# Optimization experiments

Hardware: AMD Instinct MI355X
Metric: run time of the kernel (lower is better)

## Reference

```python
import jax, jax.numpy as jnp
from jax import lax
import numpy as np

B = 32  # batch


def _conv(x, w, b, pad):
    # x: [B,Cin,H,W], w: [Cout,Cin,kh,kw], b: [Cout]
    y = lax.conv_general_dilated(x, w, window_strides=(1, 1), padding=pad,
                                 dimension_numbers=("NCHW", "OIHW", "NCHW"))
    return y + b[None, :, None, None]


def setup_inputs() -> dict:
    keys = jax.random.split(jax.random.key(0), 16)
    ki = iter(keys)
    f32 = jnp.float32

    def W(shape):
        return jax.random.normal(next(ki), shape, f32) * 0.05

    return {
        "x": jax.random.normal(next(ki), (B, 64, 64), f32),
        # 64 independent spatial convs per stage, each Conv2d(Cin,31,(64,3))
        "W1": W((64, 31, 1, 64, 3)),  "b1": jnp.zeros((64, 31), f32),
        "W2": W((64, 31, 31, 64, 3)), "b2": jnp.zeros((64, 31), f32),
        "W3": W((64, 31, 31, 64, 3)), "b3": jnp.zeros((64, 31), f32),
        # 2 edge spectral stacks: Conv(2,64,9)->ReLU->Conv(64,32,1)->ReLU->Conv(32,1,5)
        "We1a": W((2, 64, 2, 9, 9)),  "be1a": jnp.zeros((2, 64), f32),
        "We1b": W((2, 32, 64, 1, 1)), "be1b": jnp.zeros((2, 32), f32),
        "We1c": W((2, 1, 32, 5, 5)),  "be1c": jnp.zeros((2, 1), f32),
        # 29 interior spectral stacks: Conv(3,64,9)->ReLU->Conv(64,32,1)->ReLU->Conv(32,1,5)
        "We2a": W((29, 64, 3, 9, 9)),  "be2a": jnp.zeros((29, 64), f32),
        "We2b": W((29, 32, 64, 1, 1)), "be2b": jnp.zeros((29, 32), f32),
        "We2c": W((29, 1, 32, 5, 5)),  "be2c": jnp.zeros((29, 1), f32),
    }


def _spatial(inp, Ws, bs):
    # inp: [B,Cin,64,64]; Ws: [64,31,Cin,64,3]; bs: [64,31]
    def one(w, b):
        return jax.nn.relu(_conv(inp, w, b, [(0, 0), (1, 1)]))  # [B,31,1,64]
    rows = jax.vmap(one)(Ws, bs)            # [64,B,31,1,64]; row i = output line i
    return jnp.transpose(rows[:, :, :, 0, :], (1, 2, 0, 3))  # [B,31,64,64]


def _spectral(xin, wa, ba, wb, bb, wc, bc):
    h = jax.nn.relu(_conv(xin, wa, ba, [(4, 4), (4, 4)]))
    h = jax.nn.relu(_conv(h, wb, bb, [(0, 0), (0, 0)]))
    return _conv(h, wc, bc, [(2, 2), (2, 2)])[:, 0]  # [B,64,64]


def reference(x, W1, b1, W2, b2, W3, b3,
              We1a, be1a, We1b, be1b, We1c, be1c,
              We2a, be2a, We2b, be2b, We2c, be2c):
    xb = x[:, None]                         # [B,1,64,64]
    s1 = _spatial(xb, W1, b1)               # [B,31,64,64]
    s2 = _spatial(s1, W2, b2)
    s3 = _spatial(s2, W3, b3)

    # edge bands 0 and 30 use 2-channel slices
    edge_in = jnp.stack([s3[:, 0:2], s3[:, 29:31]])   # [2,B,2,64,64]
    edge = jax.vmap(_spectral)(edge_in, We1a, be1a, We1b, be1b, We1c, be1c)  # [2,B,64,64]

    # interior bands 1..29 use sliding 3-channel slices
    idx = jnp.arange(29)[:, None] + jnp.arange(3)[None, :]  # [29,3]
    mid_in = jnp.transpose(s3[:, idx], (1, 0, 2, 3, 4))     # [29,B,3,64,64]
    mid = jax.vmap(_spectral)(mid_in, We2a, be2a, We2b, be2b, We2c, be2c)  # [29,B,64,64]

    recon = jnp.concatenate(
        [edge[0][:, None], jnp.transpose(mid, (1, 0, 2, 3)), edge[1][:, None]], axis=1)
    out = s3 + recon                        # [B,31,64,64]
    # torch: .transpose(3,1).transpose(2,1) == permute(0,2,3,1)
    return jnp.transpose(out, (0, 2, 3, 1))  # [B,64,64,31]
```

## Files before the change

### kernel.cpp

```cpp
#include <hip/hip_runtime.h>
#include <hip/hip_bf16.h>
#include <stdint.h>

typedef unsigned short u16;
typedef unsigned int   u32;
typedef __attribute__((ext_vector_type(8))) short bf16x8;
typedef __attribute__((ext_vector_type(4))) float f32x4;

__device__ __forceinline__ float us2f(u16 u){ return __uint_as_float(((u32)u)<<16); }
__device__ __forceinline__ float lo2f(u32 w){ return __uint_as_float(w<<16); }
__device__ __forceinline__ float hi2f(u32 w){ return __uint_as_float(w & 0xffff0000u); }
__device__ __forceinline__ u16 f2us(float f){
  u32 u = __float_as_uint(f);
  u32 r = (u + 0x7FFFu + ((u>>16)&1u)) >> 16;
  return (u16)r;
}
__device__ __forceinline__ u32 pk2(float a, float b){ return (u32)f2us(a) | ((u32)f2us(b)<<16); }

__global__ __launch_bounds__(256) void k_prep_x(const float* __restrict__ x, u16* __restrict__ xT){
  __shared__ float tile[64][65];
  const int b = blockIdx.x, t = threadIdx.x;
  #pragma unroll
  for (int q=0;q<4;q++){
    int idx = q*256 + t, r = idx>>4, w4 = (idx&15)*4;
    float4 v = *(const float4*)&x[((size_t)b*64 + r)*64 + w4];
    tile[r][w4]=v.x; tile[r][w4+1]=v.y; tile[r][w4+2]=v.z; tile[r][w4+3]=v.w;
  }
  __syncthreads();
  #pragma unroll
  for (int q=0;q<2;q++){
    int idx = q*256 + t, w = idx>>3, rc = idx&7;
    uint4 o;
    o.x = pk2(tile[rc*8+0][w], tile[rc*8+1][w]);
    o.y = pk2(tile[rc*8+2][w], tile[rc*8+3][w]);
    o.z = pk2(tile[rc*8+4][w], tile[rc*8+5][w]);
    o.w = pk2(tile[rc*8+6][w], tile[rc*8+7][w]);
    *(uint4*)&xT[((size_t)b*64 + w)*64 + rc*8] = o;
  }
}

__global__ __launch_bounds__(256) void k_prep_w(const float* __restrict__ W,
        u16* __restrict__ Wp, int CI){
  __shared__ float rowW[5952];
  const int h = blockIdx.x, i = blockIdx.y, t = threadIdx.x;
  for (int idx=t; idx<1488; idx+=256){
    int o = idx/48, j4 = (idx - o*48)*4;
    float4 v = *(const float4*)&W[ (((size_t)h*31 + o)*CI + i)*192 + j4 ];
    *(float4*)&rowW[o*192 + j4] = v;
  }
  __syncthreads();
  for (int idx=t; idx<768; idx+=256){
    int dw = idx>>8, rem = idx&255, o = rem>>3, rc = rem&7;
    uint4 ov = {0,0,0,0};
    if (o < 31){
      const float* s = &rowW[o*192 + dw];
      ov.x = pk2(s[(rc*8+0)*3], s[(rc*8+1)*3]);
      ov.y = pk2(s[(rc*8+2)*3], s[(rc*8+3)*3]);
      ov.z = pk2(s[(rc*8+4)*3], s[(rc*8+5)*3]);
      ov.w = pk2(s[(rc*8+6)*3], s[(rc*8+7)*3]);
    }
    *(uint4*)&Wp[ ((((size_t)h*CI + i)*3 + dw)*32 + o)*64 + rc*8 ] = ov;
  }
}

__global__ __launch_bounds__(256) void k_tr(const u16* __restrict__ in, u16* __restrict__ outp){
  __shared__ u16 tile[64*72];
  const int b = blockIdx.x, o = blockIdx.y, t = threadIdx.x;
  const uint4* src = (const uint4*)(in + ((size_t)b*31 + o)*4096);
  #pragma unroll
  for (int q=0;q<2;q++){
    int idx = q*256 + t, hh = idx>>3, u = idx&7;
    *(uint4*)&tile[hh*72 + ((u ^ ((hh>>3)&7))*8)] = src[idx];
  }
  __syncthreads();
  u16* dst = outp + ((size_t)b*31 + o)*4096;
  #pragma unroll
  for (int q=0;q<2;q++){
    int idx = q*256 + t, w = idx>>3, hc = (idx&7)*8;
    u32 ow[4];
    #pragma unroll
    for (int j=0;j<4;j++){
      int h0 = hc + j*2, h1 = h0 + 1;
      u16 a = tile[h0*72 + (((w>>3) ^ ((h0>>3)&7))*8) + (w&7)];
      u16 bb= tile[h1*72 + (((w>>3) ^ ((h1>>3)&7))*8) + (w&7)];
      ow[j] = (u32)a | ((u32)bb<<16);
    }
    uint4 ov = {ow[0], ow[1], ow[2], ow[3]};
    *(uint4*)&dst[(size_t)w*64 + hc] = ov;
  }
}

__global__ __launch_bounds__(512) void k_spatial2(const u16* __restrict__ inT_g,
        const u16* __restrict__ Wp, const float* __restrict__ bias,
        float* __restrict__ outF, u16* __restrict__ outT, int CI, int mode){
  __shared__ __align__(16) u16 inT[2][66*72];
  const int t    = threadIdx.x;
  const int wv   = t>>6;
  const int lane = t&63;
  const int l15  = lane&15;
  const int quad = lane>>4;
  const int wg  = blockIdx.x;
  const int xcd = wg & 7;
  const int li  = wg >> 3;
  const int hg  = xcd*2 + (li>>5);
  const int b   = li & 31;
  const int h   = hg*4 + (wv&3);
  const int nho = wv>>2;

  if (t < 72){
    inT[0][t] = 0; inT[0][65*72 + t] = 0;
    inT[1][t] = 0; inT[1][65*72 + t] = 0;
  }

  f32x4 acc[4];
  #pragma unroll
  for (int ms=0;ms<4;ms++) acc[ms] = (f32x4){0.f,0.f,0.f,0.f};

  const uint4* srcb = (const uint4*)(inT_g + (size_t)b*CI*4096);
  const u16*   wr   = Wp + (size_t)h*CI*3*32*64;

  uint4 pf = srcb[t];
  bf16x8 bA[2][3], bB[2][3];
  #pragma unroll
  for (int dw=0;dw<3;dw++)
    #pragma unroll
    for (int kh=0;kh<2;kh++)
      bA[kh][dw] = *(const bf16x8*)&wr[(dw*32 + nho*16 + l15)*64 + kh*32 + quad*8];

  auto body = [&](bf16x8 (&bcur)[2][3], bf16x8 (&bnext)[2][3], int i){
    u16* L = inT[i&1];
    {
      int row = t>>3, ch = t&7;
      *(uint4*)&L[(row+1)*72 + ch*8] = pf;
    }
    int inext = (i+1 < CI) ? (i+1) : (CI-1);
    pf = (srcb + (size_t)inext*512)[t];
    const u16* wbase = wr + (size_t)inext*6144;
    #pragma unroll
    for (int dw=0;dw<3;dw++)
      #pragma unroll
      for (int kh=0;kh<2;kh++)
        bnext[kh][dw] = *(const bf16x8*)&wbase[(dw*32 + nho*16 + l15)*64 + kh*32 + quad*8];
    asm volatile("s_waitcnt lgkmcnt(0)" ::: "memory");
    __builtin_amdgcn_s_barrier();
    __builtin_amdgcn_sched_barrier(0);
    #pragma unroll
    for (int kh=0; kh<2; kh++){
      #pragma unroll
      for (int dw=0; dw<3; dw++){
        bf16x8 afr[4];
        #pragma unroll
        for (int ms=0;ms<4;ms++)
          afr[ms] = *(const bf16x8*)&L[(ms*16 + l15 + dw)*72 + kh*32 + quad*8];
        #pragma unroll
        for (int ms=0;ms<4;ms++)
          acc[ms] = __builtin_amdgcn_mfma_f32_16x16x32_bf16(afr[ms], bcur[kh][dw], acc[ms], 0,0,0);
      }
    }
  };

  int i = 0;
  while (true){
    body(bA, bB, i); if (++i >= CI) break;
    body(bB, bA, i); if (++i >= CI) break;
  }

  {
    int o = nho*16 + l15;
    if (o < 31){
      float bv = bias[h*31 + o];
      if (mode == 0){
        #pragma unroll
        for (int ms=0;ms<4;ms++){
          size_t base = (((size_t)b*31 + o)*64 + h)*64 + ms*16 + quad*4;
          #pragma unroll
          for (int reg=0;reg<4;reg++)
            outF[base + reg] = fmaxf(acc[ms][reg] + bv, 0.f);
        }
      } else {
        #pragma unroll
        for (int ms=0;ms<4;ms++){
          uint2 pw;
          pw.x = pk2(fmaxf(acc[ms][0] + bv, 0.f), fmaxf(acc[ms][1] + bv, 0.f));
          pw.y = pk2(fmaxf(acc[ms][2] + bv, 0.f), fmaxf(acc[ms][3] + bv, 0.f));
          *(uint2*)&outT[ (((size_t)b*31 + o)*64 + h)*64 + ms*16 + quad*4 ] = pw;
        }
      }
    }
  }
}

__global__ __launch_bounds__(256) void k_prep(
    const float* __restrict__ We1a, const float* __restrict__ We2a,
    const float* __restrict__ We1b, const float* __restrict__ We2b,
    u16* __restrict__ waP, u16* __restrict__ wbP){
  int t = blockIdx.x*256 + threadIdx.x;
  if (t < 17856){
    int g = t/576, rem = t - g*576, dx = rem>>6, c = rem&63;
    int C; const float* wa;
    if (g==0)      { C=2; wa = We1a; }
    else if (g==30){ C=2; wa = We1a + 64*2*81; }
    else           { C=3; wa = We2a + (size_t)(g-1)*64*3*81; }
    const float* wrow = wa + (size_t)c*C*81;
    u16* dst = waP + ((size_t)(g*9 + dx)*64 + c)*40;
    int Kr = C*9;
    for (int k=0;k<40;k++){
      u16 v = 0;
      if (k < Kr) v = f2us(wrow[k*9 + dx]);
      dst[k] = v;
    }
  } else if (t < 17856 + 992){
    int u = t - 17856; int g = u>>5, c2 = u&31;
    const float* wb;
    if (g==0)      wb = We1b;
    else if (g==30) wb = We1b + 32*64;
    else            wb = We2b + (size_t)(g-1)*32*64;
    u16* dst = wbP + ((size_t)g*32 + c2)*72;
    for (int k=0;k<64;k++) dst[k] = f2us(wb[c2*64 + k]);
    for (int k=64;k<72;k++) dst[k] = 0;
  }
}

__global__ __launch_bounds__(256) void k_spec_ab(
    const float* __restrict__ s3,
    const u16* __restrict__ waP, const u16* __restrict__ wbP,
    const float* __restrict__ be1a, const float* __restrict__ be1b,
    const float* __restrict__ be2a, const float* __restrict__ be2b,
    u16* __restrict__ hb, int g0){
  __shared__ __align__(16) unsigned char smem[36864];
  u16* colT  = (u16*)smem;
  u16* stage = (u16*)(smem + 23040);
  u16* haT   = (u16*)smem;
  u16* hbL   = (u16*)smem;

  const int t = threadIdx.x;
  const int yo = blockIdx.x, b = blockIdx.y;
  const int gl = blockIdx.z;
  const int g  = g0 + gl;
  const int y0 = yo*4;
  const int wv = t>>6, lane = t&63, l15 = lane&15, quad = lane>>4;

  int C, cb; const float *ba, *bb;
  if (g==0)      { C=2; cb=0;  ba=be1a;           bb=be1b;        }
  else if (g==30){ C=2; cb=29; ba=be1a+64;        bb=be1b+32;     }
  else           { C=3; cb=g-1; ba=be2a+(size_t)(g-1)*64; bb=be2b+(size_t)(g-1)*32; }

  if (t < 160){
    int yl = t/40, rem = t - yl*40, xi = rem/5, q = rem - xi*5;
    int xc = (xi < 4) ? xi : xi + 64;
    *(uint4*)&colT[(yl*72 + xc)*40 + q*8] = (uint4){0,0,0,0};
  }
  for (int idx=t; idx<576; idx+=256){
    int i = idx/192, rem = idx-192*i, yext = rem>>4, x4 = rem&15;
    int yrow = y0 + yext - 4;
    uint2 sv = {0,0};
    if (i < C && yrow >= 0 && yrow < 64){
      float4 v = *(const float4*)&s3[ (((size_t)b*31 + cb + i)*64 + yrow)*64 + x4*4 ];
      sv.x = pk2(v.x, v.y);
      sv.y = pk2(v.z, v.w);
    }
    *(uint2*)&stage[(i*12 + yext)*64 + x4*4] = sv;
  }
  __syncthreads();

  {
    const int yl = t>>6, x = t&63;
    const int C9 = C*9;
    u32 wbuf[20];
    #pragma unroll
    for (int kk=0;kk<20;kk++){
      int k0 = kk*2, k1 = kk*2+1;
      int i0 = k0/9, dy0 = k0 - i0*9;
      int i1 = k1/9, dy1 = k1 - i1*9;
      int ii0 = (k0 < C9) ? i0 : 0;
      int ii1 = (k1 < C9) ? i1 : 0;
      u32 v0 = (k0 < C9) ? (u32)stage[(ii0*12 + (yl+dy0))*64 + x] : 0u;
      u32 v1 = (k1 < C9) ? (u32)stage[(ii1*12 + (yl+dy1))*64 + x] : 0u;
      wbuf[kk] = v0 | (v1<<16);
    }
    u16* dst = &colT[(yl*72 + x + 4)*40];
    #pragma unroll
    for (int q=0;q<5;q++){
      uint4 ov = { wbuf[q*4], wbuf[q*4+1], wbuf[q*4+2], wbuf[q*4+3] };
      *(uint4*)&dst[q*8] = ov;
    }
  }
  __syncthreads();

  f32x4 acc[4][4];
  #pragma unroll
  for (int yl=0;yl<4;yl++)
    #pragma unroll
    for (int nf=0;nf<4;nf++) acc[yl][nf] = (f32x4){0.f,0.f,0.f,0.f};

  const u16* waPg = waP + (size_t)g*9*64*40;
  #pragma unroll
  for (int dx=0; dx<9; dx++){
    bf16x8 af[4];
    #pragma unroll
    for (int yl=0;yl<4;yl++)
      af[yl] = *(const bf16x8*)&colT[(yl*72 + wv*16 + l15 + dx)*40 + quad*8];
    #pragma unroll
    for (int nf=0;nf<4;nf++){
      bf16x8 bfr = *(const bf16x8*)&waPg[(dx*64 + nf*16 + l15)*40 + quad*8];
      #pragma unroll
      for (int yl=0;yl<4;yl++)
        acc[yl][nf] = __builtin_amdgcn_mfma_f32_16x16x32_bf16(af[yl], bfr, acc[yl][nf], 0,0,0);
    }
  }
  __syncthreads();

  #pragma unroll
  for (int nf=0;nf<4;nf++){
    float bav = ba[nf*16 + l15];
    #pragma unroll
    for (int yl=0;yl<4;yl++){
      int px = yl*64 + wv*16 + quad*4;
      #pragma unroll
      for (int reg=0;reg<4;reg++)
        haT[(px+reg)*72 + nf*16 + l15] = f2us(fmaxf(acc[yl][nf][reg] + bav, 0.f));
    }
  }
  __syncthreads();

  bf16x8 a2[2][4];
  #pragma unroll
  for (int kh=0; kh<2; kh++)
    #pragma unroll
    for (int j=0;j<4;j++)
      a2[kh][j] = *(const bf16x8*)&haT[((wv*4+j)*16 + l15)*72 + kh*32 + quad*8];
  __syncthreads();

  const u16* wb_g = wbP + (size_t)g*32*72;
  f32x4 acc2[4][2];
  #pragma unroll
  for (int j=0;j<4;j++){ acc2[j][0] = (f32x4){0.f,0.f,0.f,0.f}; acc2[j][1] = (f32x4){0.f,0.f,0.f,0.f}; }
  #pragma unroll
  for (int kh=0; kh<2; kh++){
    #pragma unroll
    for (int nf=0;nf<2;nf++){
      bf16x8 b2 = *(const bf16x8*)&wb_g[(nf*16 + l15)*72 + kh*32 + quad*8];
      #pragma unroll
      for (int j=0;j<4;j++)
        acc2[j][nf] = __builtin_amdgcn_mfma_f32_16x16x32_bf16(a2[kh][j], b2, acc2[j][nf], 0,0,0);
    }
  }
  #pragma unroll
  for (int nf=0;nf<2;nf++){
    float bbv = bb[nf*16 + l15];
    #pragma unroll
    for (int j=0;j<4;j++){
      int px = (wv*4+j)*16 + quad*4;
      uint2 pw;
      pw.x = pk2(fmaxf(acc2[j][nf][0] + bbv, 0.f), fmaxf(acc2[j][nf][1] + bbv, 0.f));
      pw.y = pk2(fmaxf(acc2[j][nf][2] + bbv, 0.f), fmaxf(acc2[j][nf][3] + bbv, 0.f));
      *(uint2*)&hbL[(nf*16+l15)*296 + px] = pw;
    }
  }
  __syncthreads();

  {
    int c2 = t>>3, xq = t&7;
    size_t base = (((size_t)gl*32 + b)*32 + c2)*4096 + (size_t)yo*256 + xq*32;
    #pragma unroll
    for (int q=0;q<4;q++)
      *(uint4*)&hb[base + q*8] = *(const uint4*)&hbL[c2*296 + xq*32 + q*8];
  }
}

__global__ __launch_bounds__(256) void k_spec_c(
    const u16* __restrict__ hb, const float* __restrict__ We1c, const float* __restrict__ be1c,
    const float* __restrict__ We2c, const float* __restrict__ be2c,
    float* __restrict__ rec, int g0){
  __shared__ __align__(16) unsigned char smemC[58368 + 3200];
  u16*   hbT  = (u16*)smemC;
  float* wcL  = (float*)(smemC + 58368);
  float* redc = (float*)smemC;
  const int t  = threadIdx.x;
  const int y0 = blockIdx.x*8;
  const int b  = blockIdx.y;
  const int gl = blockIdx.z;
  const int g  = g0 + gl;
  const float *wc, *bc;
  if (g==0)      { wc = We1c;             bc = be1c;       }
  else if (g==30){ wc = We1c + 800;       bc = be1c + 1;   }
  else           { wc = We2c + (g-1)*800; bc = be2c + (g-1); }

  for (int idx=t; idx<384; idx+=256){
    int c2 = idx/12, row = idx - c2*12;
    u32* d32 = (u32*)&hbT[(size_t)(c2*12 + row)*76];
    d32[0]  = 0;
    d32[33] = 0;
    u32* di = d32 + 1;
    int yg = y0 - 2 + row;
    if (yg >= 0 && yg < 64){
      const uint4* srcp = (const uint4*)&hb[ (((size_t)gl*32 + b)*32 + c2)*4096 + (size_t)yg*64 ];
      #pragma unroll
      for (int q=0;q<8;q++){
        uint4 v = srcp[q];
        di[q*4+0]=v.x; di[q*4+1]=v.y; di[q*4+2]=v.z; di[q*4+3]=v.w;
      }
    } else {
      #pragma unroll
      for (int q=0;q<32;q++) di[q] = 0;
    }
  }
  for (int idx=t; idx<800; idx+=256) wcL[idx] = wc[idx];
  __syncthreads();

  const int xt = t&7, yq = (t>>3)&7, cqt = t>>6;
  const int x0 = xt*8;
  float acc[8];
  #pragma unroll
  for (int p=0;p<8;p++) acc[p]=0.f;
  for (int c2 = cqt*8; c2 < cqt*8+8; c2++){
    #pragma unroll
    for (int dy=0;dy<5;dy++){
      const uint2* hp = (const uint2*)&hbT[(c2*12 + yq+dy)*76 + x0];
      uint2 v0 = hp[0], v1 = hp[1], v2 = hp[2];
      float h[12];
      h[0]=lo2f(v0.x); h[1]=hi2f(v0.x); h[2]=lo2f(v0.y); h[3]=hi2f(v0.y);
      h[4]=lo2f(v1.x); h[5]=hi2f(v1.x); h[6]=lo2f(v1.y); h[7]=hi2f(v1.y);
      h[8]=lo2f(v2.x); h[9]=hi2f(v2.x); h[10]=lo2f(v2.y); h[11]=hi2f(v2.y);
      #pragma unroll
      for (int dx=0;dx<5;dx++){
        float wv = wcL[c2*25 + dy*5 + dx];
        #pragma unroll
        for (int p=0;p<8;p++) acc[p] = fmaf(h[p+dx], wv, acc[p]);
      }
    }
  }
  __syncthreads();
  int slot = yq*8 + xt;
  if (cqt >= 2){
    #pragma unroll
    for (int p=0;p<8;p++) redc[((cqt-2)*64 + slot)*8 + p] = acc[p];
  }
  __syncthreads();
  if (cqt < 2){
    #pragma unroll
    for (int p=0;p<8;p++) acc[p] += redc[(cqt*64 + slot)*8 + p];
  }
  __syncthreads();
  if (cqt == 1){
    #pragma unroll
    for (int p=0;p<8;p++) redc[slot*8 + p] = acc[p];
  }
  __syncthreads();
  if (cqt == 0){
    float bcv = bc[0];
    size_t base = (((size_t)g*32 + b)*64 + (y0+yq))*64 + x0;
    #pragma unroll
    for (int p=0;p<8;p++) rec[base+p] = acc[p] + redc[slot*8 + p] + bcv;
  }
}

__global__ __launch_bounds__(256) void k_final(const float* __restrict__ s3,
        const float* __restrict__ rec, float* __restrict__ out){
  __shared__ float tile[31][65];
  const int t = threadIdx.x;
  const int y = blockIdx.x & 63;
  const int b = blockIdx.x >> 6;
  for (int idx=t; idx<1984; idx+=256){
    int o = idx>>6, x = idx&63;
    tile[o][x] = s3[ (((size_t)b*31+o)*64 + y)*64 + x ]
               + rec[ (((size_t)o*32+b)*64 + y)*64 + x ];
  }
  __syncthreads();
  size_t base = ((size_t)b*4096 + (size_t)y*64)*31;
  for (int idx=t; idx<1984; idx+=256){
    int x = idx/31, o = idx-31*x;
    out[base+idx] = tile[o][x];
  }
}

extern "C" void kernel_launch(void* const* d_in, const int* in_sizes, int n_in,
                              void* d_out, int out_size, void* d_ws, size_t ws_size,
                              hipStream_t stream){
  const float* x    = (const float*)d_in[0];
  const float* W1   = (const float*)d_in[1];
  const float* b1   = (const float*)d_in[2];
  const float* W2   = (const float*)d_in[3];
  const float* b2   = (const float*)d_in[4];
  const float* W3   = (const float*)d_in[5];
  const float* b3   = (const float*)d_in[6];
  const float* We1a = (const float*)d_in[7];
  const float* be1a = (const float*)d_in[8];
  const float* We1b = (const float*)d_in[9];
  const float* be1b = (const float*)d_in[10];
  const float* We1c = (const float*)d_in[11];
  const float* be1c = (const float*)d_in[12];
  const float* We2a = (const float*)d_in[13];
  const float* be2a = (const float*)d_in[14];
  const float* We2b = (const float*)d_in[15];
  const float* be2b = (const float*)d_in[16];
  const float* We2c = (const float*)d_in[17];
  const float* be2c = (const float*)d_in[18];
  float* out = (float*)d_out;

  char* ws = (char*)d_ws;
  float* s3  = (float*)(ws);
  u16*   Wp  = (u16*)(ws + 16777216);
  u16*   xT  = (u16*)(ws + 44040192);
  float* rec = (float*)(ws + 16777216);
  u16*   hb  = (u16*)(ws + 33030144);

  u16* bufA = (u16*)((char*)d_out);
  u16* bufB = (u16*)((char*)d_out + 8126464);
  u16* waP = (u16*)((char*)d_out);
  u16* wbP = (u16*)((char*)d_out + 1440000);

  dim3 bs(256);
  dim3 gsp(512), bsp(512), gtr(32,31);
  k_prep_x<<<dim3(32),bs,0,stream>>>(x, xT);
  k_prep_w<<<dim3(64,1),bs,0,stream>>>(W1, Wp, 1);
  k_spatial2<<<gsp,bsp,0,stream>>>(xT,  Wp, b1, nullptr, bufA, 1, 1);
  k_tr<<<gtr,bs,0,stream>>>(bufA, bufB);
  k_prep_w<<<dim3(64,31),bs,0,stream>>>(W2, Wp, 31);
  k_spatial2<<<gsp,bsp,0,stream>>>(bufB, Wp, b2, nullptr, bufA, 31, 1);
  k_tr<<<gtr,bs,0,stream>>>(bufA, bufB);
  k_prep_w<<<dim3(64,31),bs,0,stream>>>(W3, Wp, 31);
  k_spatial2<<<gsp,bsp,0,stream>>>(bufB, Wp, b3, s3, nullptr, 31, 0);

  k_prep<<<dim3(74),bs,0,stream>>>(We1a, We2a, We1b, We2b, waP, wbP);

  int batch = 8;
  if (ws_size > 33030144ull){
    size_t m = (ws_size - 33030144ull) / 8388608ull;
    if (m < 1) m = 1;
    if (m > 8) m = 8;
    batch = (int)m;
  }
  for (int g0=0; g0<31; g0+=batch){
    int c = 31 - g0; if (c > batch) c = batch;
    k_spec_ab<<<dim3(16,32,c),bs,0,stream>>>(s3, waP, wbP, be1a, be1b, be2a, be2b, hb, g0);
    k_spec_c <<<dim3(8,32,c),bs,0,stream>>>(hb, We1c,be1c,We2c,be2c, rec, g0);
  }
  k_final<<<dim3(2048),bs,0,stream>>>(s3, rec, out);
}
```

Before: 957.5 us.

## Switch spatial conv to 32x32x16 MFMA tiles and drop weight double-buffering

The spatial convolution kernel now uses the 32x32x16 bf16 MFMA instruction, so each wave computes a 32-width by 32-output-channel tile instead of four 16x16 tiles. The split across waves moves from output-channel halves to width halves. Weight fragments are now loaded at the top of each input-channel iteration rather than prefetched one iteration ahead. The larger tile is meant to cut LDS A-fragment reads and raise MFMA efficiency per instruction, but removing the weight prefetch may expose global-load latency before the MFMAs. The output stores for the fp32 path are also widened to float4.

New measurement: 1.100 ms. +14.9%, slower.

```diff
diff --git a/kernel.cpp b/kernel.cpp
--- a/kernel.cpp
+++ b/kernel.cpp
@@ -6,6 +6,7 @@
 typedef unsigned int   u32;
 typedef __attribute__((ext_vector_type(8))) short bf16x8;
 typedef __attribute__((ext_vector_type(4))) float f32x4;
+typedef __attribute__((ext_vector_type(16))) float f32x16;
 
 __device__ __forceinline__ float us2f(u16 u){ return __uint_as_float(((u32)u)<<16); }
 __device__ __forceinline__ float lo2f(u32 w){ return __uint_as_float(w<<16); }
@@ -97,37 +98,36 @@
   const int t    = threadIdx.x;
   const int wv   = t>>6;
   const int lane = t&63;
-  const int l15  = lane&15;
-  const int quad = lane>>4;
+  const int l31  = lane&31;
+  const int hi   = lane>>5;
   const int wg  = blockIdx.x;
   const int xcd = wg & 7;
   const int li  = wg >> 3;
   const int hg  = xcd*2 + (li>>5);
   const int b   = li & 31;
   const int h   = hg*4 + (wv&3);
-  const int nho = wv>>2;
+  const int wt  = wv>>2;
 
   if (t < 72){
     inT[0][t] = 0; inT[0][65*72 + t] = 0;
     inT[1][t] = 0; inT[1][65*72 + t] = 0;
   }
 
-  f32x4 acc[4];
-  #pragma unroll
-  for (int ms=0;ms<4;ms++) acc[ms] = (f32x4){0.f,0.f,0.f,0.f};
+  f32x16 acc = {0.f,0.f,0.f,0.f,0.f,0.f,0.f,0.f,0.f,0.f,0.f,0.f,0.f,0.f,0.f,0.f};
 
   const uint4* srcb = (const uint4*)(inT_g + (size_t)b*CI*4096);
   const u16*   wr   = Wp + (size_t)h*CI*3*32*64;
 
   uint4 pf = srcb[t];
-  bf16x8 bA[2][3], bB[2][3];
-  #pragma unroll
-  for (int dw=0;dw<3;dw++)
-    #pragma unroll
-    for (int kh=0;kh<2;kh++)
-      bA[kh][dw] = *(const bf16x8*)&wr[(dw*32 + nho*16 + l15)*64 + kh*32 + quad*8];
-
-  auto body = [&](bf16x8 (&bcur)[2][3], bf16x8 (&bnext)[2][3], int i){
+
+  for (int i=0;i<CI;i++){
+    const u16* wbase = wr + (size_t)i*6144;
+    bf16x8 bw[3][4];
+    #pragma unroll
+    for (int dw=0;dw<3;dw++)
+      #pragma unroll
+      for (int ks=0;ks<4;ks++)
+        bw[dw][ks] = *(const bf16x8*)&wbase[(dw*32 + l31)*64 + ks*16 + hi*8];
     u16* L = inT[i&1];
     {
       int row = t>>3, ch = t&7;
@@ -135,55 +135,42 @@
     }
     int inext = (i+1 < CI) ? (i+1) : (CI-1);
     pf = (srcb + (size_t)inext*512)[t];
-    const u16* wbase = wr + (size_t)inext*6144;
-    #pragma unroll
-    for (int dw=0;dw<3;dw++)
-      #pragma unroll
-      for (int kh=0;kh<2;kh++)
-        bnext[kh][dw] = *(const bf16x8*)&wbase[(dw*32 + nho*16 + l15)*64 + kh*32 + quad*8];
     asm volatile("s_waitcnt lgkmcnt(0)" ::: "memory");
     __builtin_amdgcn_s_barrier();
     __builtin_amdgcn_sched_barrier(0);
     #pragma unroll
-    for (int kh=0; kh<2; kh++){
-      #pragma unroll
-      for (int dw=0; dw<3; dw++){
-        bf16x8 afr[4];
-        #pragma unroll
-        for (int ms=0;ms<4;ms++)
-          afr[ms] = *(const bf16x8*)&L[(ms*16 + l15 + dw)*72 + kh*32 + quad*8];
-        #pragma unroll
-        for (int ms=0;ms<4;ms++)
-          acc[ms] = __builtin_amdgcn_mfma_f32_16x16x32_bf16(afr[ms], bcur[kh][dw], acc[ms], 0,0,0);
+    for (int dw=0; dw<3; dw++){
+      #pragma unroll
+      for (int ks=0; ks<4; ks++){
+        bf16x8 af = *(const bf16x8*)&L[(wt*32 + l31 + dw)*72 + ks*16 + hi*8];
+        acc = __builtin_amdgcn_mfma_f32_32x32x16_bf16(af, bw[dw][ks], acc, 0,0,0);
       }
     }
-  };
-
-  int i = 0;
-  while (true){
-    body(bA, bB, i); if (++i >= CI) break;
-    body(bB, bA, i); if (++i >= CI) break;
   }
 
   {
-    int o = nho*16 + l15;
+    int o = l31;
     if (o < 31){
       float bv = bias[h*31 + o];
       if (mode == 0){
         #pragma unroll
-        for (int ms=0;ms<4;ms++){
-          size_t base = (((size_t)b*31 + o)*64 + h)*64 + ms*16 + quad*4;
-          #pragma unroll
-          for (int reg=0;reg<4;reg++)
-            outF[base + reg] = fmaxf(acc[ms][reg] + bv, 0.f);
+        for (int rg=0; rg<4; rg++){
+          int w0 = wt*32 + 8*rg + 4*hi;
+          float4 v;
+          v.x = fmaxf(acc[rg*4+0] + bv, 0.f);
+          v.y = fmaxf(acc[rg*4+1] + bv, 0.f);
+          v.z = fmaxf(acc[rg*4+2] + bv, 0.f);
+          v.w = fmaxf(acc[rg*4+3] + bv, 0.f);
+          *(float4*)&outF[ (((size_t)b*31 + o)*64 + h)*64 + w0 ] = v;
         }
       } else {
         #pragma unroll
-        for (int ms=0;ms<4;ms++){
+        for (int rg=0; rg<4; rg++){
+          int w0 = wt*32 + 8*rg + 4*hi;
           uint2 pw;
-          pw.x = pk2(fmaxf(acc[ms][0] + bv, 0.f), fmaxf(acc[ms][1] + bv, 0.f));
-          pw.y = pk2(fmaxf(acc[ms][2] + bv, 0.f), fmaxf(acc[ms][3] + bv, 0.f));
-          *(uint2*)&outT[ (((size_t)b*31 + o)*64 + h)*64 + ms*16 + quad*4 ] = pw;
+          pw.x = pk2(fmaxf(acc[rg*4+0] + bv, 0.f), fmaxf(acc[rg*4+1] + bv, 0.f));
+          pw.y = pk2(fmaxf(acc[rg*4+2] + bv, 0.f), fmaxf(acc[rg*4+3] + bv, 0.f));
+          *(uint2*)&outT[ (((size_t)b*31 + o)*64 + h)*64 + w0 ] = pw;
         }
       }
     }
```
